# Kernel optimization log

Hardware: AMD Instinct MI355X
Metric: run time of the kernel (lower is better)

Reference implementation:

```python
import jax, jax.numpy as jnp
import numpy as np

B, T, C = 2, 2048, 1024
H, D = 16, 64
EPS = 1e-05
SCALE = 1.0 / np.sqrt(D)


def _rmsnorm(x, w):
    # normalize over last dim (head_dim)
    return w * (x * jax.lax.rsqrt(jnp.mean(x * x, axis=-1, keepdims=True) + EPS))


def setup_inputs() -> dict:
    key = jax.random.key(0)
    ks = jax.random.split(key, 8)
    x = jax.random.normal(ks[0], (B, T, C), dtype=jnp.float32)
    # causal mask, 1 = attend, 0 = masked
    attention_mask = jnp.tril(jnp.ones((T, T), dtype=jnp.int32))[None, None]
    s = 1.0 / np.sqrt(C)
    Wq = jax.random.normal(ks[1], (C, H * D), dtype=jnp.float32) * s
    Wk = jax.random.normal(ks[2], (C, H * D), dtype=jnp.float32) * s
    Wv = jax.random.normal(ks[3], (C, H * D), dtype=jnp.float32) * s
    Wo = jax.random.normal(ks[4], (H * D, C), dtype=jnp.float32) * s
    q_norm_w = jnp.ones((D,), dtype=jnp.float32)
    k_norm_w = jnp.ones((D,), dtype=jnp.float32)
    gate = jnp.ones((1, H, 1, 1), dtype=jnp.float32)
    return {"x": x, "attention_mask": attention_mask, "Wq": Wq, "Wk": Wk,
            "Wv": Wv, "Wo": Wo, "q_norm_w": q_norm_w, "k_norm_w": k_norm_w,
            "gate": gate}


def reference(x, attention_mask, Wq, Wk, Wv, Wo, q_norm_w, k_norm_w, gate):
    Bx, Tx, Cx = x.shape
    vx = x @ Wv                                   # [B,T,H*D] (kept for value residual)
    q = (x @ Wq).reshape(Bx, Tx, H, D).transpose(0, 2, 1, 3)  # [B,H,T,D]
    k = (x @ Wk).reshape(Bx, Tx, H, D).transpose(0, 2, 1, 3)
    v = vx.reshape(Bx, Tx, H, D).transpose(0, 2, 1, 3)
    q = _rmsnorm(q, q_norm_w)
    k = _rmsnorm(k, k_norm_w)
    att = jnp.einsum('bhqd,bhkd->bhqk', q, k) * SCALE
    att = jnp.where(attention_mask == 0, -jnp.inf, att)
    att = jax.nn.softmax(att, axis=-1)
    att = att * gate                              # per-head gating after softmax
    out = jnp.einsum('bhqk,bhkd->bhqd', att, v)
    out = out.transpose(0, 2, 1, 3).reshape(Bx, Tx, Cx)
    out = out + vx                                # value residual
    out = out @ Wo
    return out
```

## Files before the change

### kernel.cpp

```cpp
#include <hip/hip_runtime.h>

#define T_SEQ 2048
#define CDIM 1024
#define NHEAD 16
#define HDIM 64
#define BATCH 2
#define EPSV 1e-5f
#define SCALE 0.125f
#define LOG2E 1.44269504088896f
#define SMAX 16.0f

typedef __attribute__((ext_vector_type(8))) short bf16x8;
typedef __attribute__((ext_vector_type(4))) float f32x4;

__device__ __forceinline__ float b2f(short s) {
  unsigned u = ((unsigned)(unsigned short)s) << 16;
  return __builtin_bit_cast(float, u);
}
__device__ __forceinline__ short f2b(float f) {
  unsigned u = __builtin_bit_cast(unsigned, f);
  unsigned r = (u + 0x7fffu + ((u >> 16) & 1u)) >> 16;
  return (short)r;
}
__device__ __forceinline__ unsigned cvt_pk_bf16(float a, float b) {
  unsigned r;
  asm("v_cvt_pk_bf16_f32 %0, %1, %2" : "=v"(r) : "v"(a), "v"(b));
  return r;
}

__device__ __forceinline__ void gld16(const void* g, void* l) {
  __builtin_amdgcn_global_load_lds((const __attribute__((address_space(1))) unsigned*)g,
                                   (__attribute__((address_space(3))) unsigned*)l, 16, 0, 0);
}

__device__ __forceinline__ int gswz(int row) { return ((row >> 1) ^ (row >> 3)) & 3; }

__device__ __forceinline__ void stage_sw(short* lds, const char* gbase, int gstride,
                                         int w, int l) {
#pragma unroll
  for (int i = 0; i < 2; ++i) {
    int chunk = w * 2048 + i * 1024 + l * 16;
    int row = chunk >> 7;
    int bir = chunk & 127;
    const char* src = gbase + (size_t)row * gstride + (bir ^ ((row & 7) << 4));
    gld16(src, (char*)lds + chunk);
  }
}
__device__ __forceinline__ void stage_q(short* lds, const char* gbase, int gstride,
                                        int w, int l) {
#pragma unroll
  for (int i = 0; i < 4; ++i) {
    int chunk = w * 4096 + i * 1024 + l * 16;
    int row = chunk >> 7;
    int bir = chunk & 127;
    const char* src = gbase + (size_t)row * gstride + (bir ^ ((row & 7) << 4));
    gld16(src, (char*)lds + chunk);
  }
}

__global__ __launch_bounds__(256) void prep(const float* __restrict__ x,
                                            const float* __restrict__ Wq,
                                            const float* __restrict__ Wk,
                                            const float* __restrict__ Wv,
                                            const float* __restrict__ Wo,
                                            short* __restrict__ xb,
                                            short* __restrict__ WT) {
  __shared__ float tile[64][65];
  const int bid = blockIdx.x;
  if (bid < 2048) {
    size_t i = ((size_t)bid * 256 + threadIdx.x) * 8;
    float4 a = *(const float4*)&x[i];
    float4 b = *(const float4*)&x[i + 4];
    short4 lo, hi;
    lo.x = f2b(a.x); lo.y = f2b(a.y); lo.z = f2b(a.z); lo.w = f2b(a.w);
    hi.x = f2b(b.x); hi.y = f2b(b.y); hi.z = f2b(b.z); hi.w = f2b(b.w);
    *(short4*)&xb[i] = lo;
    *(short4*)&xb[i + 4] = hi;
    return;
  }
  const int t = bid - 2048;
  const int z = t >> 8, rem = t & 255;
  const float* W = (z == 0) ? Wq : (z == 1) ? Wk : (z == 2) ? Wv : Wo;
  const int r0 = (rem >> 4) * 64, c0 = (rem & 15) * 64;
  const int tr = threadIdx.x >> 4, tc4 = (threadIdx.x & 15) * 4;
#pragma unroll
  for (int i = 0; i < 4; ++i) {
    float4 v = *(const float4*)&W[(size_t)(r0 + tr + i * 16) * 1024 + c0 + tc4];
    tile[tr + i * 16][tc4 + 0] = v.x;
    tile[tr + i * 16][tc4 + 1] = v.y;
    tile[tr + i * 16][tc4 + 2] = v.z;
    tile[tr + i * 16][tc4 + 3] = v.w;
  }
  __syncthreads();
#pragma unroll
  for (int i = 0; i < 4; ++i) {
    int n = tr + i * 16;
    short4 o;
    o.x = f2b(tile[tc4 + 0][n]);
    o.y = f2b(tile[tc4 + 1][n]);
    o.z = f2b(tile[tc4 + 2][n]);
    o.w = f2b(tile[tc4 + 3][n]);
    *(short4*)&WT[((size_t)(z * 1024) + c0 + n) * 1024 + r0 + tc4] = o;
  }
}

template <int BN, bool F32OUT, bool NORM>
__global__ __launch_bounds__(256) void gemm_bf16(const short* __restrict__ A,
                                                 const short* __restrict__ Bt,
                                                 void* __restrict__ Cv,
                                                 const float* __restrict__ qw,
                                                 const float* __restrict__ kw,
                                                 int M, int N, int K, int nbx) {
  constexpr int NFR = BN / 32;
  constexpr int BITERS = BN / 64;
  __shared__ __attribute__((aligned(16))) short As[3][4096];
  __shared__ __attribute__((aligned(16))) short Bs[3][BN * 32];
  const int tid = threadIdx.x;
  const int w = tid >> 6, l = tid & 63;
  const int g = l >> 4, c = l & 15;
  const int wm = w >> 1, wn = w & 1;
  const int xcd = blockIdx.x & 7;
  const int i = blockIdx.x >> 3;
  const int bx = i >> 2;
  const int by = xcd * 4 + (i & 3);
  const int m0 = by * 128, n0 = bx * BN;
  const char* Ab = (const char*)A;
  const char* Bb = (const char*)Bt;

  auto stage = [&](int k0, int buf) {
#pragma unroll
    for (int ii = 0; ii < 2; ++ii) {
      int ci = w * 128 + ii * 64 + l;
      int row = ci >> 2, c4 = ci & 3;
      gld16(Ab + ((size_t)(m0 + row) * K + k0) * 2 + ((c4 ^ gswz(row)) << 4),
            (char*)As[buf] + (w * 2048 + ii * 1024));
    }
#pragma unroll
    for (int ii = 0; ii < BITERS; ++ii) {
      int ci = w * (64 * BITERS) + ii * 64 + l;
      int row = ci >> 2, c4 = ci & 3;
      gld16(Bb + ((size_t)(n0 + row) * K + k0) * 2 + ((c4 ^ gswz(row)) << 4),
            (char*)Bs[buf] + (w * (1024 * BITERS) + ii * 1024));
    }
  };

  f32x4 acc[4][NFR];
#pragma unroll
  for (int mt = 0; mt < 4; ++mt)
#pragma unroll
    for (int nt = 0; nt < NFR; ++nt) {
      f32x4 z = {0.f, 0.f, 0.f, 0.f};
      acc[mt][nt] = z;
    }

  const int NT = K >> 5;
  stage(0, 0);
  stage(32, 1);
  if constexpr (BITERS == 2) asm volatile("s_waitcnt vmcnt(4)" ::: "memory");
  else                       asm volatile("s_waitcnt vmcnt(3)" ::: "memory");
  __builtin_amdgcn_s_barrier();
  __builtin_amdgcn_sched_barrier(0);

  int cbuf = 0;
  for (int t = 0; t < NT; ++t) {
    int tgt = cbuf + 2; if (tgt >= 3) tgt -= 3;
    if (t + 2 < NT) stage((t + 2) << 5, tgt);
    bf16x8 a[4], bf[NFR];
#pragma unroll
    for (int mt = 0; mt < 4; ++mt) {
      const int row = wm * 64 + mt * 16 + c;
      a[mt] = *(const bf16x8*)&As[cbuf][row * 32 + ((g ^ gswz(row)) << 3)];
    }
#pragma unroll
    for (int nt = 0; nt < NFR; ++nt) {
      const int row = wn * (BN / 2) + nt * 16 + c;
      bf[nt] = *(const bf16x8*)&Bs[cbuf][row * 32 + ((g ^ gswz(row)) << 3)];
    }
    __builtin_amdgcn_s_setprio(1);
#pragma unroll
    for (int mt = 0; mt < 4; ++mt)
#pragma unroll
      for (int nt = 0; nt < NFR; ++nt)
        acc[mt][nt] = __builtin_amdgcn_mfma_f32_16x16x32_bf16(a[mt], bf[nt], acc[mt][nt], 0, 0, 0);
    __builtin_amdgcn_s_setprio(0);
    if (t + 1 < NT) {
      if (t + 2 < NT) {
        if constexpr (BITERS == 2) asm volatile("s_waitcnt vmcnt(4)" ::: "memory");
        else                       asm volatile("s_waitcnt vmcnt(3)" ::: "memory");
      } else {
        asm volatile("s_waitcnt vmcnt(0)" ::: "memory");
      }
      __builtin_amdgcn_s_barrier();
      __builtin_amdgcn_sched_barrier(0);
    }
    cbuf = cbuf + 1; if (cbuf >= 3) cbuf -= 3;
  }

  if constexpr (NORM) {
    if (n0 < 2048) {
      const float* wgt = (n0 < 1024) ? qw : kw;
      const float scl = (n0 < 1024) ? SCALE * LOG2E : 1.f;
      float w4[NFR];
#pragma unroll
      for (int nt = 0; nt < NFR; ++nt) w4[nt] = wgt[nt * 16 + c] * scl;
#pragma unroll
      for (int mt = 0; mt < 4; ++mt)
#pragma unroll
        for (int r = 0; r < 4; ++r) {
          float s = 0.f;
#pragma unroll
          for (int nt = 0; nt < NFR; ++nt) s += acc[mt][nt][r] * acc[mt][nt][r];
          s += __shfl_xor(s, 1);
          s += __shfl_xor(s, 2);
          s += __shfl_xor(s, 4);
          s += __shfl_xor(s, 8);
          const float rstd = rsqrtf(s * (1.0f / 64.0f) + EPSV);
#pragma unroll
          for (int nt = 0; nt < NFR; ++nt) acc[mt][nt][r] *= rstd * w4[nt];
        }
    }
  }

  if constexpr (F32OUT) {
    float* C = (float*)Cv;
#pragma unroll
    for (int mt = 0; mt < 4; ++mt)
#pragma unroll
      for (int nt = 0; nt < NFR; ++nt)
#pragma unroll
        for (int r = 0; r < 4; ++r)
          C[(size_t)(m0 + wm * 64 + mt * 16 + 4 * g + r) * N + n0 + wn * (BN / 2) + nt * 16 + c] =
              acc[mt][nt][r];
  } else {
    short* C = (short*)Cv;
#pragma unroll
    for (int mt = 0; mt < 4; ++mt)
#pragma unroll
      for (int nt = 0; nt < NFR; ++nt)
#pragma unroll
        for (int r = 0; r < 4; ++r)
          C[(size_t)(m0 + wm * 64 + mt * 16 + 4 * g + r) * N + n0 + wn * (BN / 2) + nt * 16 + c] =
              f2b(acc[mt][nt][r]);
  }
}

__global__ __launch_bounds__(256) void vt_kernel(const short* __restrict__ QKV,
                                                 short* __restrict__ VT) {
  __shared__ short tile[64][66];
  const int t0 = blockIdx.x * 64;
  const int h = blockIdx.y, b = blockIdx.z;
  const int tid = threadIdx.x;
  const int r = tid >> 3, c8 = (tid & 7) * 8;
#pragma unroll
  for (int p = 0; p < 2; ++p) {
    int row = r + p * 32;
    bf16x8 v = *(const bf16x8*)&QKV[(size_t)(b * T_SEQ + t0 + row) * 3072 + 2048 + h * 64 + c8];
#pragma unroll
    for (int j = 0; j < 8; ++j) tile[row][c8 + j] = v[j];
  }
  __syncthreads();
#pragma unroll
  for (int p = 0; p < 2; ++p) {
    int d = r + p * 32;
    short o[8];
#pragma unroll
    for (int j = 0; j < 8; ++j) o[j] = tile[c8 + j][d];
    *(bf16x8*)&VT[((size_t)(b * NHEAD + h) * 64 + d) * T_SEQ + t0 + c8] = *(bf16x8*)o;
  }
}

__global__ __launch_bounds__(256, 2) void attn_fwd(const short* __restrict__ QKV,
                                                   const short* __restrict__ VT,
                                                   const float* __restrict__ gate,
                                                   short* __restrict__ Ob) {
  __shared__ __attribute__((aligned(16))) short pool[40960];

  const int bid = blockIdx.x;
  const int xcd = bid & 7, s = bid >> 3;
  const int t8 = (s >> 2) & 7;
  const int Q16 = (s < 32) ? 15 - t8 : t8;
  const int bh = xcd * 4 + (s & 3);
  const int h = bh & 15, b = bh >> 4;
  const int q0 = Q16 * 128;
  const int nkt = 2 * Q16 + 2;
  const int tid = threadIdx.x;
  const int w = tid >> 6, l = tid & 63;
  const int g = l >> 4, c = l & 15;

  const char* qkb = (const char*)QKV;
  const char* kbase = qkb + ((size_t)(b * T_SEQ) * 3072 + 1024 + h * 64) * 2;
  const char* vtb = (const char*)VT + ((size_t)(b * NHEAD + h) * 64) * T_SEQ * 2;
  const float gh = gate[h];

  stage_q(pool, qkb + ((size_t)(b * T_SEQ + q0) * 3072 + h * 64) * 2, 3072 * 2, w, l);
  stage_sw(pool + 8192, kbase, 3072 * 2, w, l);
  stage_sw(pool + 24576, vtb, T_SEQ * 2, w, l);
  stage_sw(pool + 8192 + 4096, kbase + (size_t)64 * 3072 * 2, 3072 * 2, w, l);
  stage_sw(pool + 24576 + 4096, vtb + (size_t)64 * 2, T_SEQ * 2, w, l);
  asm volatile("s_waitcnt vmcnt(8)" ::: "memory");
  __builtin_amdgcn_sched_barrier(0);

  bf16x8 qf[2][2];
#pragma unroll
  for (int st = 0; st < 2; ++st) {
    const int row = w * 32 + st * 16 + c;
#pragma unroll
    for (int ks = 0; ks < 2; ++ks)
      qf[st][ks] = *(const bf16x8*)&pool[row * 64 + ((ks * 32 + g * 8) ^ ((row & 7) << 3))];
  }

  const char* poolb = (const char*)pool;
  const int bc = (c >> 2) & 1;
  const int swz_g = (g ^ (c & 3)) << 4;
  const int kvoff[2] = {c * 128 + swz_g + (bc << 6),
                        c * 128 + swz_g + ((1 ^ bc) << 6)};
  int pboff[2][2], p_off[2][4];
  const int cc = (c >> 1) & 3;
  const int pinv0 = c * 128 + ((g & 1) << 3) + ((((g >> 1) ^ c) & 1) << 4);
#pragma unroll
  for (int st = 0; st < 2; ++st) {
    const int sbase = w * 4096 + st * 2048;
#pragma unroll
    for (int ks = 0; ks < 2; ++ks) pboff[st][ks] = sbase + kvoff[ks];
#pragma unroll
    for (int mt = 0; mt < 4; ++mt) p_off[st][mt] = sbase + pinv0 + ((mt ^ cc) << 5);
  }

  bf16x8 onesf;
#pragma unroll
  for (int j = 0; j < 8; ++j) onesf[j] = (short)0x3F80;

  f32x4 oacc[2][4];
#pragma unroll
  for (int st = 0; st < 2; ++st)
#pragma unroll
    for (int dt = 0; dt < 4; ++dt) {
      f32x4 z = {0.f, 0.f, 0.f, 0.f};
      oacc[st][dt] = z;
    }
  f32x4 oacc4[2];
#pragma unroll
  for (int st = 0; st < 2; ++st) {
    f32x4 z = {0.f, 0.f, 0.f, 0.f};
    oacc4[st] = z;
  }

#define ATTN_TILE(BUF_, KT_)                                                              \
  {                                                                                       \
    constexpr int BUF = (BUF_);                                                           \
    const int kt = (KT_);                                                                 \
    const int dqw = q0 + w * 32 - kt * 64;        \
    if (dqw + 16 > -16) {                                                                 \
      f32x4 sacc[2][4];                                                                   \
      _Pragma("unroll") for (int st = 0; st < 2; ++st)                                    \
        _Pragma("unroll") for (int mt = 0; mt < 4; ++mt) {                                \
          f32x4 z = {-SMAX, -SMAX, -SMAX, -SMAX};                                         \
          sacc[st][mt] = z;                                                               \
        }                                                                                 \
      __builtin_amdgcn_s_setprio(1);                                                      \
      _Pragma("unroll") for (int mt = 0; mt < 4; ++mt) {                                  \
        _Pragma("unroll") for (int ks = 0; ks < 2; ++ks) {                                \
          bf16x8 kf = *(const bf16x8*)(poolb + 16384 + BUF * 8192 + mt * 2048 +           \
                                       kvoff[ks]);                                        \
          _Pragma("unroll") for (int st = 0; st < 2; ++st)                                \
            sacc[st][mt] = __builtin_amdgcn_mfma_f32_16x16x32_bf16(kf, qf[st][ks],        \
                                                                   sacc[st][mt], 0, 0, 0);\
        }                                                                                 \
      }                                                                                   \
      __builtin_amdgcn_s_setprio(0);                                                      \
      bf16x8 vf[4][2];                                                                    \
      _Pragma("unroll") for (int dt = 0; dt < 4; ++dt)                                    \
        _Pragma("unroll") for (int ks = 0; ks < 2; ++ks)                                  \
          vf[dt][ks] = *(const bf16x8*)(poolb + 49152 + BUF * 8192 + dt * 2048 +          \
                                        kvoff[ks]);                                       \
      _Pragma("unroll") for (int st = 0; st < 2; ++st) {                                  \
        const int dqs = dqw + st * 16;                                                    \
        if (dqs < 63) {                                                                   \
          _Pragma("unroll") for (int mt = 0; mt < 4; ++mt)                                \
            _Pragma("unroll") for (int r = 0; r < 4; ++r)                                 \
              if (mt * 16 + 4 * g + r > dqs + c) sacc[st][mt][r] = -1e30f;                \
        }                                                                                 \
        _Pragma("unroll") for (int mt = 0; mt < 4; ++mt) {                                \
          float p0 = exp2f(sacc[st][mt][0]);                                              \
          float p1 = exp2f(sacc[st][mt][1]);                                              \
          float p2 = exp2f(sacc[st][mt][2]);                                              \
          float p3 = exp2f(sacc[st][mt][3]);                                              \
          uint2 pk;                                                                       \
          pk.x = cvt_pk_bf16(p0, p1);                                                     \
          pk.y = cvt_pk_bf16(p2, p3);                                                     \
          *(uint2*)((char*)pool + p_off[st][mt]) = pk;                                    \
        }                                                                                 \
      }                                                                                   \
      bf16x8 pb[2][2];                                                                    \
      _Pragma("unroll") for (int st = 0; st < 2; ++st)                                    \
        _Pragma("unroll") for (int ks = 0; ks < 2; ++ks)                                  \
          pb[st][ks] = *(const bf16x8*)(poolb + pboff[st][ks]);                           \
      __builtin_amdgcn_s_setprio(1);                                                      \
      _Pragma("unroll") for (int dt = 0; dt < 4; ++dt)                                    \
        _Pragma("unroll") for (int ks = 0; ks < 2; ++ks)                                  \
          _Pragma("unroll") for (int st = 0; st < 2; ++st)                                \
            oacc[st][dt] = __builtin_amdgcn_mfma_f32_16x16x32_bf16(vf[dt][ks],            \
                                                                   pb[st][ks],           \
                                                                   oacc[st][dt], 0, 0, 0);\
      _Pragma("unroll") for (int st = 0; st < 2; ++st) {                                  \
        oacc4[st] = __builtin_amdgcn_mfma_f32_16x16x32_bf16(onesf, pb[st][0],             \
                                                            oacc4[st], 0, 0, 0);          \
        oacc4[st] = __builtin_amdgcn_mfma_f32_16x16x32_bf16(onesf, pb[st][1],             \
                                                            oacc4[st], 0, 0, 0);          \
      }                                                                                   \
      __builtin_amdgcn_s_setprio(0);                                                      \
    }                                                                                     \
  }

#define ATTN_PAIR(B_, T0_)                                                                \
  {                                                                                       \
    constexpr int PB = (B_);                                                              \
    const int pt0 = (T0_);                                                                \
    asm volatile("s_waitcnt vmcnt(0)" ::: "memory");                                      \
    __builtin_amdgcn_s_barrier();                                                         \
    __builtin_amdgcn_sched_barrier(0);                                                    \
    if (pt0 + 2 < nkt) {                                                                  \
      constexpr int TB = PB ^ 2;                                                          \
      stage_sw(pool + 8192 + TB * 4096, kbase + (size_t)(pt0 + 2) * 64 * 3072 * 2,        \
               3072 * 2, w, l);                                                           \
      stage_sw(pool + 24576 + TB * 4096, vtb + (size_t)(pt0 + 2) * 64 * 2,                \
               T_SEQ * 2, w, l);                                                          \
      stage_sw(pool + 8192 + (TB + 1) * 4096, kbase + (size_t)(pt0 + 3) * 64 * 3072 * 2,  \
               3072 * 2, w, l);                                                           \
      stage_sw(pool + 24576 + (TB + 1) * 4096, vtb + (size_t)(pt0 + 3) * 64 * 2,          \
               T_SEQ * 2, w, l);                                                          \
    }                                                                                     \
    ATTN_TILE(PB, pt0);                                                                   \
    ATTN_TILE(PB + 1, pt0 + 1);                                                           \
  }

  int t0 = 0;
  for (; t0 + 4 <= nkt; t0 += 4) {
    ATTN_PAIR(0, t0);
    ATTN_PAIR(2, t0 + 2);
  }
  if (t0 < nkt) ATTN_PAIR(0, t0);
#undef ATTN_PAIR
#undef ATTN_TILE

#pragma unroll
  for (int st = 0; st < 2; ++st) {
    const float gl = gh / oacc4[st][0];
    const int qrow = q0 + w * 32 + st * 16 + c;
    const short* Vr = QKV + (size_t)(b * T_SEQ + qrow) * 3072 + 2048 + h * 64;
    short* Oro = Ob + (size_t)(b * T_SEQ + qrow) * 1024 + h * 64;
#pragma unroll
    for (int dt = 0; dt < 4; ++dt) {
      const int d0 = dt * 16 + 4 * g;
      short4 vres = *(const short4*)&Vr[d0];
      short4 o;
      o.x = f2b(oacc[st][dt][0] * gl + b2f(vres.x));
      o.y = f2b(oacc[st][dt][1] * gl + b2f(vres.y));
      o.z = f2b(oacc[st][dt][2] * gl + b2f(vres.z));
      o.w = f2b(oacc[st][dt][3] * gl + b2f(vres.w));
      *(short4*)&Oro[d0] = o;
    }
  }
}

extern "C" void kernel_launch(void* const* d_in, const int* in_sizes, int n_in,
                              void* d_out, int out_size, void* d_ws, size_t ws_size,
                              hipStream_t stream) {
  const float* x  = (const float*)d_in[0];
  const float* Wq = (const float*)d_in[2];
  const float* Wk = (const float*)d_in[3];
  const float* Wv = (const float*)d_in[4];
  const float* Wo = (const float*)d_in[5];
  const float* qw = (const float*)d_in[6];
  const float* kw = (const float*)d_in[7];
  const float* gate = (const float*)d_in[8];
  float* out = (float*)d_out;

  char* ws = (char*)d_ws;
  short* xb  = (short*)ws;
  short* WT  = (short*)(ws + ((size_t)8 << 20));
  short* QKV = (short*)(ws + ((size_t)16 << 20));
  short* VTb = (short*)(ws + ((size_t)40 << 20));
  short* Obf = (short*)(ws + ((size_t)48 << 20));

  const int M = BATCH * T_SEQ;

  prep<<<3072, 256, 0, stream>>>(x, Wq, Wk, Wv, Wo, xb, WT);
  gemm_bf16<128, false, true><<<768, 256, 0, stream>>>(xb, WT, QKV, qw, kw, M, 3072, CDIM, 24);
  vt_kernel<<<dim3(32, 16, 2), 256, 0, stream>>>(QKV, VTb);
  attn_fwd<<<512, 256, 0, stream>>>(QKV, VTb, gate, Obf);
  gemm_bf16<64, true, false><<<512, 256, 0, stream>>>(Obf, WT + (size_t)3072 * 1024, out,
                                                      nullptr, nullptr, M, CDIM, CDIM, 16);
}
```

Baseline: 117.9 us.

## Switch attention K/V staging to a three-buffer per-tile ring with partial waits

Replaces the four-buffer pair-wise K/V prefetch scheme with a three-slot ring, where each tile waits only for its own loads (vmcnt(4)) and issues the prefetch two tiles ahead. Shared memory per block drops from 80KB to 64KB, which may let more blocks fit per CU, and the wait no longer drains every outstanding load. In exchange it adds a barrier per tile instead of per pair, and correctness depends on the vmcnt accounting matching the number of loads stage_sw issues.

```diff
diff --git a/kernel.cpp b/kernel.cpp
--- a/kernel.cpp
+++ b/kernel.cpp
@@ -273,7 +273,7 @@
                                                    const short* __restrict__ VT,
                                                    const float* __restrict__ gate,
                                                    short* __restrict__ Ob) {
-  __shared__ __attribute__((aligned(16))) short pool[40960];
+  __shared__ __attribute__((aligned(16))) short pool[32768];
 
   const int bid = blockIdx.x;
   const int xcd = bid & 7, s = bid >> 3;
@@ -294,9 +294,9 @@
 
   stage_q(pool, qkb + ((size_t)(b * T_SEQ + q0) * 3072 + h * 64) * 2, 3072 * 2, w, l);
   stage_sw(pool + 8192, kbase, 3072 * 2, w, l);
-  stage_sw(pool + 24576, vtb, T_SEQ * 2, w, l);
+  stage_sw(pool + 20480, vtb, T_SEQ * 2, w, l);
   stage_sw(pool + 8192 + 4096, kbase + (size_t)64 * 3072 * 2, 3072 * 2, w, l);
-  stage_sw(pool + 24576 + 4096, vtb + (size_t)64 * 2, T_SEQ * 2, w, l);
+  stage_sw(pool + 20480 + 4096, vtb + (size_t)64 * 2, T_SEQ * 2, w, l);
   asm volatile("s_waitcnt vmcnt(8)" ::: "memory");
   __builtin_amdgcn_sched_barrier(0);
 
@@ -345,10 +345,21 @@
     oacc4[st] = z;
   }
 
-#define ATTN_TILE(BUF_, KT_)                                                              \
+#define ATTN_BODY(BUF_, KT_)                                                              \
   {                                                                                       \
     constexpr int BUF = (BUF_);                                                           \
     const int kt = (KT_);                                                                 \
+    if (kt + 1 < nkt) asm volatile("s_waitcnt vmcnt(4)" ::: "memory");                    \
+    else              asm volatile("s_waitcnt vmcnt(0)" ::: "memory");                    \
+    __builtin_amdgcn_s_barrier();                                                         \
+    __builtin_amdgcn_sched_barrier(0);                                                    \
+    if (kt + 2 < nkt) {                                                                   \
+      constexpr int TGT = (BUF + 2) % 3;                                                  \
+      stage_sw(pool + 8192 + TGT * 4096, kbase + (size_t)(kt + 2) * 64 * 3072 * 2,        \
+               3072 * 2, w, l);                                                           \
+      stage_sw(pool + 20480 + TGT * 4096, vtb + (size_t)(kt + 2) * 64 * 2,                \
+               T_SEQ * 2, w, l);                                                          \
+    }                                                                                     \
     const int dqw = q0 + w * 32 - kt * 64;        \
     if (dqw + 16 > -16) {                                                                 \
       f32x4 sacc[2][4];                                                                   \
@@ -371,7 +382,7 @@
       bf16x8 vf[4][2];                                                                    \
       _Pragma("unroll") for (int dt = 0; dt < 4; ++dt)                                    \
         _Pragma("unroll") for (int ks = 0; ks < 2; ++ks)                                  \
-          vf[dt][ks] = *(const bf16x8*)(poolb + 49152 + BUF * 8192 + dt * 2048 +          \
+          vf[dt][ks] = *(const bf16x8*)(poolb + 40960 + BUF * 8192 + dt * 2048 +          \
                                         kvoff[ks]);                                       \
       _Pragma("unroll") for (int st = 0; st < 2; ++st) {                                  \
         const int dqs = dqw + st * 16;                                                    \
@@ -412,36 +423,15 @@
     }                                                                                     \
   }
 
-#define ATTN_PAIR(B_, T0_)                                                                \
-  {                                                                                       \
-    constexpr int PB = (B_);                                                              \
-    const int pt0 = (T0_);                                                                \
-    asm volatile("s_waitcnt vmcnt(0)" ::: "memory");                                      \
-    __builtin_amdgcn_s_barrier();                                                         \
-    __builtin_amdgcn_sched_barrier(0);                                                    \
-    if (pt0 + 2 < nkt) {                                                                  \
-      constexpr int TB = PB ^ 2;                                                          \
-      stage_sw(pool + 8192 + TB * 4096, kbase + (size_t)(pt0 + 2) * 64 * 3072 * 2,        \
-               3072 * 2, w, l);                                                           \
-      stage_sw(pool + 24576 + TB * 4096, vtb + (size_t)(pt0 + 2) * 64 * 2,                \
-               T_SEQ * 2, w, l);                                                          \
-      stage_sw(pool + 8192 + (TB + 1) * 4096, kbase + (size_t)(pt0 + 3) * 64 * 3072 * 2,  \
-               3072 * 2, w, l);                                                           \
-      stage_sw(pool + 24576 + (TB + 1) * 4096, vtb + (size_t)(pt0 + 3) * 64 * 2,          \
-               T_SEQ * 2, w, l);                                                          \
-    }                                                                                     \
-    ATTN_TILE(PB, pt0);                                                                   \
-    ATTN_TILE(PB + 1, pt0 + 1);                                                           \
-  }
-
-  int t0 = 0;
-  for (; t0 + 4 <= nkt; t0 += 4) {
-    ATTN_PAIR(0, t0);
-    ATTN_PAIR(2, t0 + 2);
-  }
-  if (t0 < nkt) ATTN_PAIR(0, t0);
-#undef ATTN_PAIR
-#undef ATTN_TILE
+  int base = 0;
+  for (; base + 3 <= nkt; base += 3) {
+    ATTN_BODY(0, base);
+    ATTN_BODY(1, base + 1);
+    ATTN_BODY(2, base + 2);
+  }
+  if (base < nkt) ATTN_BODY(0, base);
+  if (base + 1 < nkt) ATTN_BODY(1, base + 1);
+#undef ATTN_BODY
 
 #pragma unroll
   for (int st = 0; st < 2; ++st) {
```

Result: no change. 117.7 us (-0.2%).
